# Kernel optimization log

Hardware: AMD Instinct MI355X
Metric: run time of the kernel (lower is better)

## Reference

```python
import jax, jax.numpy as jnp
import numpy as np
import math

B, S, D = 4, 4096, 1024
H, HD, LK = 16, 64, 256


def setup_inputs() -> dict:
    key = jax.random.key(0)
    ks = jax.random.split(key, 8)
    s = 1.0 / math.sqrt(D)
    return {
        "X": jax.random.normal(ks[0], (B, S, D), jnp.float32),
        "mask": jnp.ones((B, S), jnp.float32),
        "Wq": jax.random.normal(ks[1], (D, H * HD), jnp.float32) * s,
        "bq": jnp.zeros((H * HD,), jnp.float32),
        "Wk": jax.random.normal(ks[2], (D, H * HD), jnp.float32) * s,
        "bk": jnp.zeros((H * HD,), jnp.float32),
        "Wv": jax.random.normal(ks[3], (D, H * HD), jnp.float32) * s,
        "bv": jnp.zeros((H * HD,), jnp.float32),
        "E": jax.random.normal(ks[4], (H, LK, S), jnp.float32) / math.sqrt(LK),
        "Wo": jax.random.normal(ks[5], (H * HD, D), jnp.float32) * s,
        "bo": jnp.zeros((D,), jnp.float32),
    }


def reference(X, mask, Wq, bq, Wk, bk, Wv, bv, E, Wo, bo):
    Bd, Sd, Dd = X.shape

    def split_heads(t):  # [B,S,H*HD] -> [B,H,S,HD]
        return t.reshape(Bd, Sd, H, HD).transpose(0, 2, 1, 3)

    Q = split_heads(X @ Wq + bq)
    K = split_heads(X @ Wk + bk)
    V = split_heads(X @ Wv + bv)

    m = mask[:, None, :, None]  # [B,1,S,1]
    # Low-rank projection along sequence: [H,LK,S] x [B,H,S,HD] -> [B,H,LK,HD]
    Kp = jnp.einsum('hks,bhsd->bhkd', E, K * m)
    Vp = jnp.einsum('hks,bhsd->bhkd', E, V * m)

    dot = jnp.einsum('bhsd,bhkd->bhsk', Q, Kp) / math.sqrt(HD)
    attn = jax.nn.softmax(dot, axis=-1)
    Xo = jnp.einsum('bhsk,bhkd->bhsd', attn, Vp)

    Xo = Xo.transpose(0, 2, 1, 3).reshape(Bd, Sd, H * HD)
    return Xo @ Wo + bo
```

## Files before the change

### kernel.cpp

```cpp
#include <hip/hip_runtime.h>
#include <hip/hip_bf16.h>
#include <stdint.h>

typedef __bf16 bf16_t;
typedef __attribute__((ext_vector_type(8))) __bf16 bf16x8;
typedef __attribute__((ext_vector_type(4))) __bf16 bf16x4;
typedef __attribute__((ext_vector_type(4))) float f32x4;

#define TO_GLB(p) ((const __attribute__((address_space(1))) void*)(p))
#define TO_LDS(p) ((__attribute__((address_space(3))) void*)(p))

__global__ __launch_bounds__(256) void cast2_bf16_kernel(const float* __restrict__ a,
                                                         bf16_t* __restrict__ da,
                                                         const float* __restrict__ b,
                                                         bf16_t* __restrict__ db, int n4) {
  int i = blockIdx.x * 256 + threadIdx.x;
  const float* s = (i < n4) ? a : b;
  bf16_t* d = (i < n4) ? da : db;
  int j = (i < n4) ? i : i - n4;
  float4 v = ((const float4*)s)[j];
  bf16x4 o;
  o[0] = (bf16_t)v.x; o[1] = (bf16_t)v.y; o[2] = (bf16_t)v.z; o[3] = (bf16_t)v.w;
  ((bf16x4*)d)[j] = o;
}

__global__ __launch_bounds__(256) void transpose_cast4(
    const float* __restrict__ W0, const float* __restrict__ W1, const float* __restrict__ W2,
    const float* __restrict__ W3, bf16_t* __restrict__ o0, bf16_t* __restrict__ o1,
    bf16_t* __restrict__ o2, bf16_t* __restrict__ o3) {
  const int RC = 1024;
  __shared__ bf16_t tile[64][72];
  int z = blockIdx.z;
  const float* W = (z == 0) ? W0 : (z == 1) ? W1 : (z == 2) ? W2 : W3;
  bf16_t* out = (z == 0) ? o0 : (z == 1) ? o1 : (z == 2) ? o2 : o3;
  int r0 = blockIdx.y * 64, c0 = blockIdx.x * 64;
  int tid = threadIdx.x;
#pragma unroll
  for (int p = 0; p < 4; ++p) {
    int r = p * 16 + (tid >> 4);
    int c = (tid & 15) * 4;
    float4 v = *(const float4*)(W + (size_t)(r0 + r) * RC + c0 + c);
    tile[r][c + 0] = (bf16_t)v.x; tile[r][c + 1] = (bf16_t)v.y;
    tile[r][c + 2] = (bf16_t)v.z; tile[r][c + 3] = (bf16_t)v.w;
  }
  __syncthreads();
#pragma unroll
  for (int p = 0; p < 4; ++p) {
    int c = p * 16 + (tid >> 4);
    int r = (tid & 15) * 4;
    bf16x4 o;
    o[0] = tile[r + 0][c]; o[1] = tile[r + 1][c];
    o[2] = tile[r + 2][c]; o[3] = tile[r + 3][c];
    *(bf16x4*)(out + (size_t)(c0 + c) * RC + r0 + r) = o;
  }
}


#define AS_(s) (GemmLds + (s) * 16384)
#define BS_(s) (GemmLds + 32768 + (s) * 16384)

#define STAGE_A(s, h, k0v)                                                                   \
  do {                                                                                       \
    _Pragma("unroll") for (int it_ = 0; it_ < 2; ++it_) {                                    \
      int brow_ = it_ * 128 + (h) * 64 + (wv << 3);                                          \
      int row_ = brow_ + (lane >> 3);                                                        \
      int cc_ = (lane & 7) ^ (lane >> 3);                                                    \
      const bf16_t* ga_ = Ab + (size_t)row_ * K + (k0v) + cc_ * 8;                           \
      __builtin_amdgcn_global_load_lds(TO_GLB(ga_), TO_LDS(AS_(s) + brow_ * 64), 16, 0, 0);  \
    }                                                                                        \
  } while (0)

#define STAGE_B(s, h, k0v)                                                                   \
  do {                                                                                       \
    _Pragma("unroll") for (int it_ = 0; it_ < 2; ++it_) {                                    \
      int brow_ = (it_ * 2 + (wv >> 2)) * 64 + (h) * 32 + ((wv & 3) << 3);                   \
      int row_ = brow_ + (lane >> 3);                                                        \
      int cc_ = (lane & 7) ^ (lane >> 3);                                                    \
      const bf16_t* gb_ = Bb + (size_t)row_ * K + (k0v) + cc_ * 8;                           \
      __builtin_amdgcn_global_load_lds(TO_GLB(gb_), TO_LDS(BS_(s) + brow_ * 64), 16, 0, 0);  \
    }                                                                                        \
  } while (0)

#define VM4 asm volatile("s_waitcnt vmcnt(4)" ::: "memory")
#define BARRIER __builtin_amdgcn_s_barrier()
#define LGKM0 asm volatile("s_waitcnt lgkmcnt(0)" ::: "memory")

#define LOAD_AF(s, mh)                                                                       \
  do {                                                                                       \
    _Pragma("unroll") for (int kk_ = 0; kk_ < 2; ++kk_)                                      \
        _Pragma("unroll") for (int t_ = 0; t_ < 4; ++t_) {                                   \
      int ra_ = wm * 128 + (mh) * 64 + t_ * 16 + m_in;                                       \
      af[kk_][t_] = *(const bf16x8*)(AS_(s) + ra_ * 64 + (((kk_ * 4 + q) ^ (ra_ & 7)) * 8)); \
    }                                                                                        \
  } while (0)

#define LOAD_BF(s, nh, dst)                                                                  \
  do {                                                                                       \
    _Pragma("unroll") for (int kk_ = 0; kk_ < 2; ++kk_)                                      \
        _Pragma("unroll") for (int n_ = 0; n_ < 2; ++n_) {                                   \
      int rb_ = wn * 64 + (nh) * 32 + n_ * 16 + m_in;                                        \
      dst[kk_][n_] = *(const bf16x8*)(BS_(s) + rb_ * 64 + (((kk_ * 4 + q) ^ (rb_ & 7)) * 8)); \
    }                                                                                        \
  } while (0)

#define MFMA_Q(mh, nh, bfr)                                                                  \
  do {                                                                                       \
    __builtin_amdgcn_s_setprio(1);                                                           \
    _Pragma("unroll") for (int kk_ = 0; kk_ < 2; ++kk_)                                      \
        _Pragma("unroll") for (int t_ = 0; t_ < 4; ++t_)                                     \
            _Pragma("unroll") for (int n_ = 0; n_ < 2; ++n_)                                 \
                acc[(mh) * 4 + t_][(nh) * 2 + n_] = __builtin_amdgcn_mfma_f32_16x16x32_bf16( \
                    af[kk_][t_], bfr[kk_][n_], acc[(mh) * 4 + t_][(nh) * 2 + n_], 0, 0, 0);  \
    __builtin_amdgcn_s_setprio(0);                                                           \
  } while (0)

#define KTILE(s, ST1, ST2, ST3, ST4)                                                         \
  do {                                                                                       \
    LOAD_AF(s, 0); LOAD_BF(s, 0, bf0);                                                       \
    ST1; BARRIER; LGKM0; MFMA_Q(0, 0, bf0); BARRIER;                                         \
    LOAD_BF(s, 1, bf1);                                                                      \
    ST2; BARRIER; LGKM0; MFMA_Q(0, 1, bf1); BARRIER;                                         \
    LOAD_AF(s, 1);                                                                           \
    ST3; BARRIER; LGKM0; MFMA_Q(1, 0, bf0); BARRIER;                                         \
    ST4; VM4; BARRIER; MFMA_Q(1, 1, bf1); BARRIER;                                           \
  } while (0)

__global__ __launch_bounds__(512, 2) void gemm_bt_8ph(
    const bf16_t* __restrict__ A, const bf16_t* __restrict__ B, int K, int mode,
    const float* __restrict__ bq, const float* __restrict__ bk, const float* __restrict__ bv,
    const float* __restrict__ mask,
    bf16_t* __restrict__ Q, bf16_t* __restrict__ KT, bf16_t* __restrict__ VT,
    const float* __restrict__ bo, float* __restrict__ out) {
  int tid = threadIdx.x;
  int lane = tid & 63, wv = tid >> 6;
  int wm = wv >> 2, wn = wv & 3;
  int q = lane >> 4, m_in = lane & 15;
  int bid = blockIdx.x;
  int bm = bid & 63, bn = bid >> 6;
  size_t m0 = (size_t)bm * 256;
  size_t n0 = (size_t)bn * 256;
  const bf16_t* Ab = A + m0 * K;
  const bf16_t* Bb = B + n0 * K;
  __shared__ __align__(16) bf16_t GemmLds[65536];

  f32x4 acc[8][4];
  bf16x8 af[2][4], bf0[2][2], bf1[2][2];
  f32x4 z = {0.f, 0.f, 0.f, 0.f};
#pragma unroll
  for (int mt = 0; mt < 8; ++mt)
#pragma unroll
    for (int nt = 0; nt < 4; ++nt) acc[mt][nt] = z;

  int NT = K >> 6;
  int NI = NT >> 1;

  STAGE_A(0, 0, 0); STAGE_B(0, 0, 0); STAGE_A(0, 1, 0); STAGE_B(0, 1, 0);
  STAGE_A(1, 0, 64); STAGE_B(1, 0, 64);
  asm volatile("s_waitcnt vmcnt(4)" ::: "memory");
  __builtin_amdgcn_s_barrier();

  for (int i = 0; i < NI; ++i) {
    int kt = 2 * i;
    int k1 = (kt + 1) * 64;
    int k2 = (kt + 2 < NT) ? (kt + 2) * 64 : 0;
    int k3 = (kt + 3 < NT) ? (kt + 3) * 64 : 0;
    KTILE(0, STAGE_A(1, 1, k1), STAGE_B(1, 1, k1), STAGE_A(0, 0, k2), STAGE_B(0, 0, k2));
    KTILE(1, STAGE_A(0, 1, k2), STAGE_B(0, 1, k2), STAGE_A(1, 0, k3), STAGE_B(1, 0, k3));
  }
  asm volatile("s_waitcnt vmcnt(0)" ::: "memory");

  if (mode == 0) {
    __syncthreads();
    int proj = (int)(n0 >> 10);
    int b = (int)(m0 >> 12), st0 = (int)(m0 & 4095);
    int nb10 = (int)(n0 & 1023);
    if (proj == 0) {
#pragma unroll
      for (int mt = 0; mt < 8; ++mt) {
#pragma unroll
        for (int nt = 0; nt < 4; ++nt) {
          int n = wn * 64 + nt * 16 + m_in;
          float bias = bq[nb10 + n];
#pragma unroll
          for (int r = 0; r < 4; ++r) {
            int tl = wm * 128 + mt * 16 + q * 4 + r;
            GemmLds[tl * 256 + ((((n >> 3) ^ (tl & 31)) << 3) | (n & 7))] =
                (bf16_t)(acc[mt][nt][r] + bias);
          }
        }
      }
      __syncthreads();
      int hb = (int)(n0 >> 6);
#pragma unroll
      for (int it = 0; it < 16; ++it) {
        int cid = it * 512 + tid;
        int tl = cid >> 5, c = cid & 31;
        bf16x8 v = *(const bf16x8*)(GemmLds + tl * 256 + ((c ^ (tl & 31)) << 3));
        int h = hb + (c >> 3);
        *(bf16x8*)(Q + ((size_t)(b * 16 + h) * 4096 + st0 + tl) * 64 + (c & 7) * 8) = v;
      }
    } else {
      bf16_t* dstb = (proj == 1) ? KT : VT;
      const float* bp = (proj == 1) ? bk : bv;
#pragma unroll
      for (int mt = 0; mt < 8; ++mt) {
        int mb = wm * 128 + mt * 16 + q * 4;
        float mk[4];
#pragma unroll
        for (int r = 0; r < 4; ++r) mk[r] = mask[b * 4096 + st0 + mb + r];
#pragma unroll
        for (int nt = 0; nt < 4; ++nt) {
          int n = wn * 64 + nt * 16 + m_in;
          float bias = bp[nb10 + n];
#pragma unroll
          for (int r = 0; r < 4; ++r) {
            int tl = mb + r;
            GemmLds[n * 256 + ((((tl >> 3) ^ (n & 31)) << 3) | (tl & 7))] =
                (bf16_t)((acc[mt][nt][r] + bias) * mk[r]);
          }
        }
      }
      __syncthreads();
#pragma unroll
      for (int it = 0; it < 16; ++it) {
        int cid = it * 512 + tid;
        int nl = cid >> 5, c = cid & 31;
        bf16x8 v = *(const bf16x8*)(GemmLds + nl * 256 + ((c ^ (nl & 31)) << 3));
        int c10 = nb10 + nl, h = c10 >> 6, hd = c10 & 63;
        *(bf16x8*)(dstb + ((size_t)(b * 16 + h) * 64 + hd) * 4096 + st0 + c * 8) = v;
      }
    }
  } else {
    float* L = (float*)GemmLds;
    __syncthreads();
#pragma unroll
    for (int hh = 0; hh < 2; ++hh) {
      if (hh) __syncthreads();
      if (wm == hh) {
#pragma unroll
        for (int mt = 0; mt < 8; ++mt) {
#pragma unroll
          for (int nt = 0; nt < 4; ++nt) {
            int n = wn * 64 + nt * 16 + m_in;
            float bias = bo[(int)n0 + n];
#pragma unroll
            for (int r = 0; r < 4; ++r) {
              int row = mt * 16 + q * 4 + r;
              L[row * 256 + (n ^ ((row & 7) << 2))] = acc[mt][nt][r] + bias;
            }
          }
        }
      }
      __syncthreads();
#pragma unroll
      for (int it = 0; it < 16; ++it) {
        int cid = it * 512 + tid;
        int row = cid >> 6, c = cid & 63;
        f32x4 v = *(const f32x4*)(L + row * 256 + ((c ^ (row & 7)) << 2));
        *(f32x4*)(out + (size_t)((int)m0 + hh * 128 + row) * 1024 + (int)n0 + c * 4) = v;
      }
    }
  }
}

__global__ __launch_bounds__(512) void gemm2_kernel(
    const bf16_t* __restrict__ E, const bf16_t* __restrict__ KT, const bf16_t* __restrict__ VT,
    float* __restrict__ Pp) {
  int tid = threadIdx.x, lane = tid & 63, wv = tid >> 6;
  int wm = wv >> 1, wn = wv & 1;
  int q = lane >> 4, m_in = lane & 15;
  int mt0 = blockIdx.x;
  int bh = blockIdx.y;
  int kc = blockIdx.z;
  int h = bh & 15;
  const bf16_t* Ab = E + (size_t)h * 256 * 4096 + (size_t)mt0 * 128 * 4096 + (size_t)kc * 2048;
  const bf16_t* BbK = KT + (size_t)bh * 64 * 4096 + (size_t)kc * 2048;
  const bf16_t* BbV = VT + (size_t)bh * 64 * 4096 + (size_t)kc * 2048;
  __shared__ __align__(16) bf16_t As[2 * 16384];
  __shared__ __align__(16) bf16_t BsK[2 * 8192];
  __shared__ __align__(16) bf16_t BsV[2 * 8192];

#define G2_STAGE(slot, k0v)                                                                   \
  do {                                                                                        \
    _Pragma("unroll") for (int it = 0; it < 4; ++it) {                                        \
      int l = it * 512 + tid;                                                                 \
      int kkb = l >> 10, row = (l >> 3) & 127, cc = (l & 7) ^ (row & 7);                      \
      const bf16_t* ga = Ab + (size_t)row * 4096 + (k0v) + kkb * 64 + cc * 8;                 \
      __builtin_amdgcn_global_load_lds(TO_GLB(ga),                                            \
          TO_LDS(As + (slot) * 16384 + (it * 512 + wv * 64) * 8), 16, 0, 0);                  \
    }                                                                                         \
    _Pragma("unroll") for (int it = 0; it < 2; ++it) {                                        \
      int l = it * 512 + tid;                                                                 \
      int kkb = l >> 9, row = (l >> 3) & 63, cc = (l & 7) ^ (row & 7);                        \
      const bf16_t* gb = BbK + (size_t)row * 4096 + (k0v) + kkb * 64 + cc * 8;                \
      __builtin_amdgcn_global_load_lds(TO_GLB(gb),                                            \
          TO_LDS(BsK + (slot) * 8192 + (it * 512 + wv * 64) * 8), 16, 0, 0);                  \
    }                                                                                         \
    _Pragma("unroll") for (int it = 0; it < 2; ++it) {                                        \
      int l = it * 512 + tid;                                                                 \
      int kkb = l >> 9, row = (l >> 3) & 63, cc = (l & 7) ^ (row & 7);                        \
      const bf16_t* gb = BbV + (size_t)row * 4096 + (k0v) + kkb * 64 + cc * 8;                \
      __builtin_amdgcn_global_load_lds(TO_GLB(gb),                                            \
          TO_LDS(BsV + (slot) * 8192 + (it * 512 + wv * 64) * 8), 16, 0, 0);                  \
    }                                                                                         \
  } while (0)

  f32x4 accK[2][2], accV[2][2];
  f32x4 z = {0.f, 0.f, 0.f, 0.f};
#pragma unroll
  for (int mt = 0; mt < 2; ++mt)
#pragma unroll
    for (int nt = 0; nt < 2; ++nt) { accK[mt][nt] = z; accV[mt][nt] = z; }

  G2_STAGE(0, 0);
  __syncthreads();

  for (int t = 0; t < 16; ++t) {
    int cur = t & 1;
    if (t < 15) G2_STAGE(cur ^ 1, (t + 1) * 128);
#pragma unroll
    for (int kk4 = 0; kk4 < 4; ++kk4) {
      int kkb = kk4 >> 1, qq = (kk4 & 1) * 4 + q;
      bf16x8 afr[2], bK[2], bV[2];
#pragma unroll
      for (int mt = 0; mt < 2; ++mt) {
        int ra = wm * 32 + mt * 16 + m_in;
        afr[mt] = *(const bf16x8*)(As + cur * 16384 + kkb * 8192 + ra * 64 + ((qq ^ (ra & 7)) * 8));
      }
#pragma unroll
      for (int nt = 0; nt < 2; ++nt) {
        int rb = wn * 32 + nt * 16 + m_in;
        bK[nt] = *(const bf16x8*)(BsK + cur * 8192 + kkb * 4096 + rb * 64 + ((qq ^ (rb & 7)) * 8));
        bV[nt] = *(const bf16x8*)(BsV + cur * 8192 + kkb * 4096 + rb * 64 + ((qq ^ (rb & 7)) * 8));
      }
#pragma unroll
      for (int mt = 0; mt < 2; ++mt)
#pragma unroll
        for (int nt = 0; nt < 2; ++nt) {
          accK[mt][nt] = __builtin_amdgcn_mfma_f32_16x16x32_bf16(afr[mt], bK[nt], accK[mt][nt], 0, 0, 0);
          accV[mt][nt] = __builtin_amdgcn_mfma_f32_16x16x32_bf16(afr[mt], bV[nt], accV[mt][nt], 0, 0, 0);
        }
    }
    __syncthreads();
  }
#undef G2_STAGE

  float* PK = Pp + ((size_t)(bh * 2 + 0) * 2 + kc) * 16384;
  float* PV = Pp + ((size_t)(bh * 2 + 1) * 2 + kc) * 16384;
#pragma unroll
  for (int mt = 0; mt < 2; ++mt) {
    int lk = mt0 * 128 + wm * 32 + mt * 16 + q * 4;
#pragma unroll
    for (int nt = 0; nt < 2; ++nt) {
      int hd = wn * 32 + nt * 16 + m_in;
#pragma unroll
      for (int r = 0; r < 4; ++r) {
        PK[(size_t)(lk + r) * 64 + hd] = accK[mt][nt][r];
        PV[(size_t)(lk + r) * 64 + hd] = accV[mt][nt][r];
      }
    }
  }
}

__global__ __launch_bounds__(256) void gemm2_reduce(const float* __restrict__ Pp,
                                                    bf16_t* __restrict__ Kp,
                                                    bf16_t* __restrict__ VpT) {
  int bh = blockIdx.x, kv = blockIdx.y;
  int tid = threadIdx.x;
  const float* P = Pp + ((size_t)(bh * 2 + kv) * 2) * 16384;
  if (kv == 0) {
#pragma unroll
    for (int it = 0; it < 16; ++it) {
      int e4 = it * 256 + tid;
      f32x4 s = *(const f32x4*)(P + e4 * 4);
      f32x4 s1 = *(const f32x4*)(P + 16384 + e4 * 4);
      s += s1;
      bf16x4 v;
#pragma unroll
      for (int r = 0; r < 4; ++r) v[r] = (bf16_t)s[r];
      *(bf16x4*)(Kp + (size_t)bh * 16384 + e4 * 4) = v;
    }
  } else {
    __shared__ __align__(16) bf16_t T[16384];
#pragma unroll
    for (int it = 0; it < 16; ++it) {
      int e4 = it * 256 + tid;
      f32x4 s = *(const f32x4*)(P + e4 * 4);
      f32x4 s1 = *(const f32x4*)(P + 16384 + e4 * 4);
      s += s1;
      int lk = (e4 * 4) >> 6, hd0 = (e4 * 4) & 63;
#pragma unroll
      for (int r = 0; r < 4; ++r) {
        int hd = hd0 + r;
        T[hd * 256 + ((((lk >> 3) ^ (hd & 31)) << 3) | (lk & 7))] = (bf16_t)s[r];
      }
    }
    __syncthreads();
#pragma unroll
    for (int it = 0; it < 8; ++it) {
      int cid = it * 256 + tid;
      int hd = cid >> 5, c = cid & 31;
      bf16x8 v = *(const bf16x8*)(T + hd * 256 + ((c ^ (hd & 31)) << 3));
      *(bf16x8*)(VpT + (size_t)bh * 16384 + hd * 256 + c * 8) = v;
    }
  }
}

__global__ __launch_bounds__(256) void attn_kernel(
    const bf16_t* __restrict__ Q, const bf16_t* __restrict__ Kp, const bf16_t* __restrict__ VpT,
    bf16_t* __restrict__ Xo) {
  int tid = threadIdx.x, lane = tid & 63, wv = tid >> 6;
  int q = lane >> 4, m_in = lane & 15;
  int s0 = blockIdx.x * 64;
  int bh = blockIdx.y;
  int b = bh >> 4, h = bh & 15;
  const bf16_t* Qb = Q + ((size_t)bh * 4096 + s0 + wv * 16) * 64;
  const bf16_t* Kpb = Kp + (size_t)bh * 16384;
  const bf16_t* Vb = VpT + (size_t)bh * 16384;
  __shared__ __align__(16) bf16_t buf[16384];

#pragma unroll
  for (int it = 0; it < 8; ++it) {
    int l = it * 256 + tid;
    int row = l >> 3, cc = (l & 7) ^ (row & 7);
    const bf16_t* g = Kpb + row * 64 + cc * 8;
    __builtin_amdgcn_global_load_lds(TO_GLB(g), TO_LDS(buf + (it * 256 + wv * 64) * 8), 16, 0, 0);
  }
  bf16x8 aq[2];
#pragma unroll
  for (int ks = 0; ks < 2; ++ks) aq[ks] = *(const bf16x8*)(Qb + (size_t)m_in * 64 + ks * 32 + q * 8);
  __syncthreads();

  f32x4 sc[16];
  f32x4 z = {0.f, 0.f, 0.f, 0.f};
#pragma unroll
  for (int nt = 0; nt < 16; ++nt) sc[nt] = z;
#pragma unroll
  for (int nt = 0; nt < 16; ++nt)
#pragma unroll
    for (int ks = 0; ks < 2; ++ks) {
      int nb = nt * 16 + m_in, qq = ks * 4 + q;
      bf16x8 kb = *(const bf16x8*)(buf + nb * 64 + ((qq ^ (nb & 7)) * 8));
      sc[nt] = __builtin_amdgcn_mfma_f32_16x16x32_bf16(aq[ks], kb, sc[nt], 0, 0, 0);
    }

  float mx[4], sm[4];
#pragma unroll
  for (int r = 0; r < 4; ++r) mx[r] = -1e30f;
#pragma unroll
  for (int nt = 0; nt < 16; ++nt)
#pragma unroll
    for (int r = 0; r < 4; ++r) {
      float t = sc[nt][r] * 0.125f;
      sc[nt][r] = t;
      mx[r] = fmaxf(mx[r], t);
    }
#pragma unroll
  for (int off = 1; off < 16; off <<= 1)
#pragma unroll
    for (int r = 0; r < 4; ++r) mx[r] = fmaxf(mx[r], __shfl_xor(mx[r], off));
#pragma unroll
  for (int r = 0; r < 4; ++r) sm[r] = 0.f;
#pragma unroll
  for (int nt = 0; nt < 16; ++nt)
#pragma unroll
    for (int r = 0; r < 4; ++r) {
      float e = __expf(sc[nt][r] - mx[r]);
      sc[nt][r] = e;
      sm[r] += e;
    }
#pragma unroll
  for (int off = 1; off < 16; off <<= 1)
#pragma unroll
    for (int r = 0; r < 4; ++r) sm[r] += __shfl_xor(sm[r], off);
  float inv[4];
#pragma unroll
  for (int r = 0; r < 4; ++r) inv[r] = 1.0f / sm[r];

  __syncthreads();

  bf16_t* Pw = buf + wv * 4096;
#pragma unroll
  for (int nt = 0; nt < 16; ++nt) {
    int cw = nt * 2 + (m_in >> 3);
#pragma unroll
    for (int r = 0; r < 4; ++r) {
      int rp = q * 4 + r;
      int sw = (((cw ^ (rp & 7)) << 3) | (m_in & 7));
      Pw[rp * 256 + sw] = (bf16_t)(sc[nt][r] * inv[r]);
    }
  }
  bf16x8 pa[8];
#pragma unroll
  for (int ks = 0; ks < 8; ++ks) {
    int c = ks * 4 + q;
    pa[ks] = *(const bf16x8*)(Pw + m_in * 256 + ((c ^ (m_in & 7)) << 3));
  }
  __syncthreads();

#pragma unroll
  for (int it = 0; it < 8; ++it) {
    int l = it * 256 + tid;
    int row = l >> 5, cc = l & 31;
    int src_cc = (cc & 24) | ((cc ^ row) & 7);
    const bf16_t* g = Vb + row * 256 + src_cc * 8;
    __builtin_amdgcn_global_load_lds(TO_GLB(g), TO_LDS(buf + (it * 256 + wv * 64) * 8), 16, 0, 0);
  }
  __syncthreads();

  f32x4 o[4];
#pragma unroll
  for (int nt = 0; nt < 4; ++nt) o[nt] = z;
#pragma unroll
  for (int nt = 0; nt < 4; ++nt)
#pragma unroll
    for (int ks = 0; ks < 8; ++ks) {
      int nb = nt * 16 + m_in, qq = ks * 4 + q;
      int p = (qq & 24) | ((qq ^ nb) & 7);
      bf16x8 vb = *(const bf16x8*)(buf + nb * 256 + p * 8);
      o[nt] = __builtin_amdgcn_mfma_f32_16x16x32_bf16(pa[ks], vb, o[nt], 0, 0, 0);
    }

#pragma unroll
  for (int nt = 0; nt < 4; ++nt)
#pragma unroll
    for (int r = 0; r < 4; ++r)
      Xo[((size_t)b * 4096 + s0 + wv * 16 + q * 4 + r) * 1024 + h * 64 + nt * 16 + m_in] =
          (bf16_t)o[nt][r];
}

extern "C" void kernel_launch(void* const* d_in, const int* in_sizes, int n_in,
                              void* d_out, int out_size, void* d_ws, size_t ws_size,
                              hipStream_t stream) {
  const float* X = (const float*)d_in[0];
  const float* mask = (const float*)d_in[1];
  const float* Wq = (const float*)d_in[2];
  const float* bq = (const float*)d_in[3];
  const float* Wk = (const float*)d_in[4];
  const float* bk = (const float*)d_in[5];
  const float* Wv = (const float*)d_in[6];
  const float* bv = (const float*)d_in[7];
  const float* E = (const float*)d_in[8];
  const float* Wo = (const float*)d_in[9];
  const float* bo = (const float*)d_in[10];
  float* out = (float*)d_out;

  char* ws = (char*)d_ws;
  const size_t SZ = 33554432;
  bf16_t* Xb = (bf16_t*)(ws);
  float* Pp = (float*)(ws);
  bf16_t* Eb = (bf16_t*)(ws + SZ);
  bf16_t* Qb = (bf16_t*)(ws + 2 * SZ);
  bf16_t* KT = (bf16_t*)(ws + 3 * SZ);
  bf16_t* VT = (bf16_t*)(ws + 4 * SZ);
  bf16_t* Kp = (bf16_t*)(ws + 5 * SZ);
  bf16_t* VpT = (bf16_t*)(ws + 5 * SZ + 8388608);
  bf16_t* WqkvT = (bf16_t*)(ws + 5 * SZ + 2 * 8388608);
  bf16_t* WoT = (bf16_t*)(ws + 5 * SZ + 2 * 8388608 + 6291456);
  bf16_t* Xo = Xb;

  cast2_bf16_kernel<<<32768, 256, 0, stream>>>(X, Xb, E, Eb, 4194304);
  transpose_cast4<<<dim3(16, 16, 4), 256, 0, stream>>>(
      Wq, Wk, Wv, Wo, WqkvT, WqkvT + 1048576, WqkvT + 2097152, WoT);

  gemm_bt_8ph<<<768, 512, 0, stream>>>(Xb, WqkvT, 1024, 0, bq, bk, bv, mask,
                                       Qb, KT, VT, nullptr, nullptr);
  gemm2_kernel<<<dim3(2, 64, 2), 512, 0, stream>>>(Eb, KT, VT, Pp);
  gemm2_reduce<<<dim3(64, 2), 256, 0, stream>>>(Pp, Kp, VpT);
  attn_kernel<<<dim3(64, 64), 256, 0, stream>>>(Qb, Kp, VpT, Xo);
  gemm_bt_8ph<<<256, 512, 0, stream>>>(Xo, WoT, 1024, 1, nullptr, nullptr, nullptr,
                                       nullptr, nullptr, nullptr, nullptr, bo, out);
}
```

Before: 452.3 us.

## Fuse split-K low-rank projection and reduce into one kernel; prefetch Vp into registers

The sequence-projection GEMM and its separate split-K reduce kernel become one kernel. Each block now covers 64 LK rows over the full 4096-long sequence, with waves split between the K and V products. It writes bf16 Kp and a transposed VpT directly through an LDS staging tile, removing the fp32 partial buffer and one launch. This halves per-block parallelism along K (256 blocks, 32 k-steps each), which may lengthen the serial chain. Separately, the attention kernel loads its Vp tile into registers early, overlapping with the QK/softmax phase, then stores it to LDS instead of doing a global-to-LDS load later.

```diff
diff --git a/kernel.cpp b/kernel.cpp
--- a/kernel.cpp
+++ b/kernel.cpp
@@ -263,146 +263,100 @@
   }
 }
 
-__global__ __launch_bounds__(512) void gemm2_kernel(
+__global__ __launch_bounds__(512) void gemm2_fused(
     const bf16_t* __restrict__ E, const bf16_t* __restrict__ KT, const bf16_t* __restrict__ VT,
-    float* __restrict__ Pp) {
+    bf16_t* __restrict__ Kp, bf16_t* __restrict__ VpT) {
   int tid = threadIdx.x, lane = tid & 63, wv = tid >> 6;
-  int wm = wv >> 1, wn = wv & 1;
+  int kvsel = wv & 1;
+  int wn2 = (wv >> 1) & 1;
+  int ws = wv >> 2;
   int q = lane >> 4, m_in = lane & 15;
   int mt0 = blockIdx.x;
   int bh = blockIdx.y;
-  int kc = blockIdx.z;
   int h = bh & 15;
-  const bf16_t* Ab = E + (size_t)h * 256 * 4096 + (size_t)mt0 * 128 * 4096 + (size_t)kc * 2048;
-  const bf16_t* BbK = KT + (size_t)bh * 64 * 4096 + (size_t)kc * 2048;
-  const bf16_t* BbV = VT + (size_t)bh * 64 * 4096 + (size_t)kc * 2048;
-  __shared__ __align__(16) bf16_t As[2 * 16384];
-  __shared__ __align__(16) bf16_t BsK[2 * 8192];
-  __shared__ __align__(16) bf16_t BsV[2 * 8192];
-
-#define G2_STAGE(slot, k0v)                                                                   \
+  const bf16_t* Ab = E + (size_t)h * 256 * 4096 + (size_t)mt0 * 64 * 4096;
+  const bf16_t* BbK = KT + (size_t)bh * 64 * 4096;
+  const bf16_t* BbV = VT + (size_t)bh * 64 * 4096;
+  __shared__ __align__(16) bf16_t G2Lds[49152];
+  bf16_t* const As = G2Lds;
+  bf16_t* const BsK = G2Lds + 16384;
+  bf16_t* const BsV = G2Lds + 32768;
+
+#define G2F_ONE(mat, base, slot, k0v)                                                         \
   do {                                                                                        \
-    _Pragma("unroll") for (int it = 0; it < 4; ++it) {                                        \
-      int l = it * 512 + tid;                                                                 \
-      int kkb = l >> 10, row = (l >> 3) & 127, cc = (l & 7) ^ (row & 7);                      \
-      const bf16_t* ga = Ab + (size_t)row * 4096 + (k0v) + kkb * 64 + cc * 8;                 \
-      __builtin_amdgcn_global_load_lds(TO_GLB(ga),                                            \
-          TO_LDS(As + (slot) * 16384 + (it * 512 + wv * 64) * 8), 16, 0, 0);                  \
-    }                                                                                         \
     _Pragma("unroll") for (int it = 0; it < 2; ++it) {                                        \
       int l = it * 512 + tid;                                                                 \
       int kkb = l >> 9, row = (l >> 3) & 63, cc = (l & 7) ^ (row & 7);                        \
-      const bf16_t* gb = BbK + (size_t)row * 4096 + (k0v) + kkb * 64 + cc * 8;                \
-      __builtin_amdgcn_global_load_lds(TO_GLB(gb),                                            \
-          TO_LDS(BsK + (slot) * 8192 + (it * 512 + wv * 64) * 8), 16, 0, 0);                  \
+      const bf16_t* g = base + (size_t)row * 4096 + (k0v) + kkb * 64 + cc * 8;                \
+      __builtin_amdgcn_global_load_lds(TO_GLB(g),                                             \
+          TO_LDS(mat + (slot) * 8192 + (it * 512 + wv * 64) * 8), 16, 0, 0);                  \
     }                                                                                         \
-    _Pragma("unroll") for (int it = 0; it < 2; ++it) {                                        \
-      int l = it * 512 + tid;                                                                 \
-      int kkb = l >> 9, row = (l >> 3) & 63, cc = (l & 7) ^ (row & 7);                        \
-      const bf16_t* gb = BbV + (size_t)row * 4096 + (k0v) + kkb * 64 + cc * 8;                \
-      __builtin_amdgcn_global_load_lds(TO_GLB(gb),                                            \
-          TO_LDS(BsV + (slot) * 8192 + (it * 512 + wv * 64) * 8), 16, 0, 0);                  \
-    }                                                                                         \
-  } while (0)
-
-  f32x4 accK[2][2], accV[2][2];
+  } while (0)
+#define G2F_STAGE(slot, k0v)                                                                  \
+  do { G2F_ONE(As, Ab, slot, k0v); G2F_ONE(BsK, BbK, slot, k0v); G2F_ONE(BsV, BbV, slot, k0v); } while (0)
+
+  f32x4 acc[2][2];
   f32x4 z = {0.f, 0.f, 0.f, 0.f};
 #pragma unroll
   for (int mt = 0; mt < 2; ++mt)
 #pragma unroll
-    for (int nt = 0; nt < 2; ++nt) { accK[mt][nt] = z; accV[mt][nt] = z; }
-
-  G2_STAGE(0, 0);
-  __syncthreads();
-
-  for (int t = 0; t < 16; ++t) {
+    for (int nt = 0; nt < 2; ++nt) acc[mt][nt] = z;
+
+  const bf16_t* Bsel = kvsel ? BsV : BsK;
+
+  G2F_STAGE(0, 0);
+  __syncthreads();
+
+  for (int t = 0; t < 32; ++t) {
     int cur = t & 1;
-    if (t < 15) G2_STAGE(cur ^ 1, (t + 1) * 128);
+    if (t < 31) G2F_STAGE(cur ^ 1, (t + 1) * 128);
 #pragma unroll
     for (int kk4 = 0; kk4 < 4; ++kk4) {
       int kkb = kk4 >> 1, qq = (kk4 & 1) * 4 + q;
-      bf16x8 afr[2], bK[2], bV[2];
+      bf16x8 afr[2], bfr[2];
 #pragma unroll
       for (int mt = 0; mt < 2; ++mt) {
-        int ra = wm * 32 + mt * 16 + m_in;
-        afr[mt] = *(const bf16x8*)(As + cur * 16384 + kkb * 8192 + ra * 64 + ((qq ^ (ra & 7)) * 8));
+        int ra = ws * 32 + mt * 16 + m_in;
+        afr[mt] = *(const bf16x8*)(As + cur * 8192 + kkb * 4096 + ra * 64 + ((qq ^ (ra & 7)) * 8));
       }
 #pragma unroll
       for (int nt = 0; nt < 2; ++nt) {
-        int rb = wn * 32 + nt * 16 + m_in;
-        bK[nt] = *(const bf16x8*)(BsK + cur * 8192 + kkb * 4096 + rb * 64 + ((qq ^ (rb & 7)) * 8));
-        bV[nt] = *(const bf16x8*)(BsV + cur * 8192 + kkb * 4096 + rb * 64 + ((qq ^ (rb & 7)) * 8));
+        int rb = wn2 * 32 + nt * 16 + m_in;
+        bfr[nt] = *(const bf16x8*)(Bsel + cur * 8192 + kkb * 4096 + rb * 64 + ((qq ^ (rb & 7)) * 8));
       }
 #pragma unroll
       for (int mt = 0; mt < 2; ++mt)
 #pragma unroll
-        for (int nt = 0; nt < 2; ++nt) {
-          accK[mt][nt] = __builtin_amdgcn_mfma_f32_16x16x32_bf16(afr[mt], bK[nt], accK[mt][nt], 0, 0, 0);
-          accV[mt][nt] = __builtin_amdgcn_mfma_f32_16x16x32_bf16(afr[mt], bV[nt], accV[mt][nt], 0, 0, 0);
-        }
+        for (int nt = 0; nt < 2; ++nt)
+          acc[mt][nt] = __builtin_amdgcn_mfma_f32_16x16x32_bf16(afr[mt], bfr[nt], acc[mt][nt], 0, 0, 0);
     }
     __syncthreads();
   }
-#undef G2_STAGE
-
-  float* PK = Pp + ((size_t)(bh * 2 + 0) * 2 + kc) * 16384;
-  float* PV = Pp + ((size_t)(bh * 2 + 1) * 2 + kc) * 16384;
+#undef G2F_STAGE
+#undef G2F_ONE
+
+  bf16_t* const TK = G2Lds;
+  bf16_t* const TV = G2Lds + 4608;
 #pragma unroll
   for (int mt = 0; mt < 2; ++mt) {
-    int lk = mt0 * 128 + wm * 32 + mt * 16 + q * 4;
 #pragma unroll
     for (int nt = 0; nt < 2; ++nt) {
-      int hd = wn * 32 + nt * 16 + m_in;
+      int hd = wn2 * 32 + nt * 16 + m_in;
 #pragma unroll
       for (int r = 0; r < 4; ++r) {
-        PK[(size_t)(lk + r) * 64 + hd] = accK[mt][nt][r];
-        PV[(size_t)(lk + r) * 64 + hd] = accV[mt][nt][r];
-      }
-    }
-  }
-}
-
-__global__ __launch_bounds__(256) void gemm2_reduce(const float* __restrict__ Pp,
-                                                    bf16_t* __restrict__ Kp,
-                                                    bf16_t* __restrict__ VpT) {
-  int bh = blockIdx.x, kv = blockIdx.y;
-  int tid = threadIdx.x;
-  const float* P = Pp + ((size_t)(bh * 2 + kv) * 2) * 16384;
-  if (kv == 0) {
-#pragma unroll
-    for (int it = 0; it < 16; ++it) {
-      int e4 = it * 256 + tid;
-      f32x4 s = *(const f32x4*)(P + e4 * 4);
-      f32x4 s1 = *(const f32x4*)(P + 16384 + e4 * 4);
-      s += s1;
-      bf16x4 v;
-#pragma unroll
-      for (int r = 0; r < 4; ++r) v[r] = (bf16_t)s[r];
-      *(bf16x4*)(Kp + (size_t)bh * 16384 + e4 * 4) = v;
-    }
-  } else {
-    __shared__ __align__(16) bf16_t T[16384];
-#pragma unroll
-    for (int it = 0; it < 16; ++it) {
-      int e4 = it * 256 + tid;
-      f32x4 s = *(const f32x4*)(P + e4 * 4);
-      f32x4 s1 = *(const f32x4*)(P + 16384 + e4 * 4);
-      s += s1;
-      int lk = (e4 * 4) >> 6, hd0 = (e4 * 4) & 63;
-#pragma unroll
-      for (int r = 0; r < 4; ++r) {
-        int hd = hd0 + r;
-        T[hd * 256 + ((((lk >> 3) ^ (hd & 31)) << 3) | (lk & 7))] = (bf16_t)s[r];
-      }
-    }
-    __syncthreads();
-#pragma unroll
-    for (int it = 0; it < 8; ++it) {
-      int cid = it * 256 + tid;
-      int hd = cid >> 5, c = cid & 31;
-      bf16x8 v = *(const bf16x8*)(T + hd * 256 + ((c ^ (hd & 31)) << 3));
-      *(bf16x8*)(VpT + (size_t)bh * 16384 + hd * 256 + c * 8) = v;
-    }
+        int lk = ws * 32 + mt * 16 + q * 4 + r;
+        if (kvsel == 0) TK[lk * 72 + hd] = (bf16_t)acc[mt][nt][r];
+        else            TV[hd * 72 + lk] = (bf16_t)acc[mt][nt][r];
+      }
+    }
+  }
+  __syncthreads();
+  {
+    int row = tid >> 3, c = tid & 7;
+    bf16x8 vK = *(const bf16x8*)(TK + row * 72 + c * 8);
+    *(bf16x8*)(Kp + (size_t)bh * 16384 + mt0 * 4096 + row * 64 + c * 8) = vK;
+    bf16x8 vV = *(const bf16x8*)(TV + row * 72 + c * 8);
+    *(bf16x8*)(VpT + (size_t)bh * 16384 + row * 256 + mt0 * 64 + c * 8) = vV;
   }
 }
 
@@ -429,6 +383,14 @@
   bf16x8 aq[2];
 #pragma unroll
   for (int ks = 0; ks < 2; ++ks) aq[ks] = *(const bf16x8*)(Qb + (size_t)m_in * 64 + ks * 32 + q * 8);
+  bf16x8 vp[8];
+#pragma unroll
+  for (int it = 0; it < 8; ++it) {
+    int l = it * 256 + tid;
+    int row = l >> 5, cc = l & 31;
+    int src_cc = (cc & 24) | ((cc ^ row) & 7);
+    vp[it] = *(const bf16x8*)(Vb + row * 256 + src_cc * 8);
+  }
   __syncthreads();
 
   f32x4 sc[16];
@@ -499,13 +461,8 @@
   __syncthreads();
 
 #pragma unroll
-  for (int it = 0; it < 8; ++it) {
-    int l = it * 256 + tid;
-    int row = l >> 5, cc = l & 31;
-    int src_cc = (cc & 24) | ((cc ^ row) & 7);
-    const bf16_t* g = Vb + row * 256 + src_cc * 8;
-    __builtin_amdgcn_global_load_lds(TO_GLB(g), TO_LDS(buf + (it * 256 + wv * 64) * 8), 16, 0, 0);
-  }
+  for (int it = 0; it < 8; ++it)
+    *(bf16x8*)(buf + (it * 256 + tid) * 8) = vp[it];
   __syncthreads();
 
   f32x4 o[4];
@@ -548,7 +505,6 @@
   char* ws = (char*)d_ws;
   const size_t SZ = 33554432;
   bf16_t* Xb = (bf16_t*)(ws);
-  float* Pp = (float*)(ws);
   bf16_t* Eb = (bf16_t*)(ws + SZ);
   bf16_t* Qb = (bf16_t*)(ws + 2 * SZ);
   bf16_t* KT = (bf16_t*)(ws + 3 * SZ);
@@ -565,8 +521,7 @@
 
   gemm_bt_8ph<<<768, 512, 0, stream>>>(Xb, WqkvT, 1024, 0, bq, bk, bv, mask,
                                        Qb, KT, VT, nullptr, nullptr);
-  gemm2_kernel<<<dim3(2, 64, 2), 512, 0, stream>>>(Eb, KT, VT, Pp);
-  gemm2_reduce<<<dim3(64, 2), 256, 0, stream>>>(Pp, Kp, VpT);
+  gemm2_fused<<<dim3(4, 64), 512, 0, stream>>>(Eb, KT, VT, Kp, VpT);
   attn_kernel<<<dim3(64, 64), 256, 0, stream>>>(Qb, Kp, VpT, Xo);
   gemm_bt_8ph<<<256, 512, 0, stream>>>(Xo, WoT, 1024, 1, nullptr, nullptr, nullptr,
                                        nullptr, nullptr, nullptr, nullptr, bo, out);
```

Result: no change. 457.0 us (+1.0%).
